# Kernel optimization log

Measured on AMD Instinct MI355X. Metric: run time of the kernel, lower is better.

The kernel has to match this reference:

```python
import jax, jax.numpy as jnp
import numpy as np

N_NODES = 10000
N_EDGES = 640000
NODE_DIM = 128
EDGE_DIM = 32
OUT_DIM = 128


def setup_inputs() -> dict:
    key = jax.random.key(0)
    k_h, k_e, k_ef, k_w1, k_w2 = jax.random.split(key, 5)
    h = jax.random.normal(k_h, (N_NODES, NODE_DIM), dtype=jnp.float32)
    edge_index = jax.random.randint(k_e, (2, N_EDGES), 0, N_NODES, dtype=jnp.int64)
    edge_features = jax.random.normal(k_ef, (N_EDGES, EDGE_DIM), dtype=jnp.float32)
    in_dim = 2 * NODE_DIM + EDGE_DIM
    # Kaiming-ish init scale for realism
    W1 = jax.random.normal(k_w1, (in_dim, OUT_DIM), dtype=jnp.float32) / np.sqrt(in_dim)
    b1 = jnp.zeros((OUT_DIM,), dtype=jnp.float32)
    W2 = jax.random.normal(k_w2, (OUT_DIM, OUT_DIM), dtype=jnp.float32) / np.sqrt(OUT_DIM)
    b2 = jnp.zeros((OUT_DIM,), dtype=jnp.float32)
    return {"h": h, "edge_index": edge_index, "edge_features": edge_features,
            "n": N_NODES, "W1": W1, "b1": b1, "W2": W2, "b2": b2}


def reference(h, edge_index, edge_features, n, W1, b1, W2, b2):
    rows, cols = edge_index[0], edge_index[1]
    # gather source/target node features + edge features -> [E, 2*node_dim+edge_dim]
    msg_input = jnp.concatenate([h[rows], h[cols], edge_features], axis=-1)
    hidden = jax.nn.relu(msg_input @ W1 + b1)   # [E, out_dim]
    messages = hidden @ W2 + b2                 # [E, out_dim]
    # scatter-add messages onto destination rows -> [n, out_dim]
    out = jax.ops.segment_sum(messages, rows, num_segments=n)
    return out
```

## Files before the change

kernel.cpp:

```cpp
#include <hip/hip_runtime.h>
#include <hip/hip_bf16.h>


typedef __attribute__((ext_vector_type(8))) short bf16x8;
typedef __attribute__((ext_vector_type(4))) float f32x4;

#define ND 128
#define ED 32
#define NL1 4096

__device__ __forceinline__ short f2bf(float x) {
  unsigned int u = __float_as_uint(x);
  unsigned int r = (u + 0x7FFFu + ((u >> 16) & 1u)) >> 16;
  return (short)r;
}

__device__ __forceinline__ float bf2f(short s) {
  return __uint_as_float(((unsigned int)(unsigned short)s) << 16);
}

__device__ __forceinline__ f32x4 bf8lo(bf16x8 v) {
  f32x4 r;
  #pragma unroll
  for (int j = 0; j < 4; ++j) r[j] = bf2f(v[j]);
  return r;
}
__device__ __forceinline__ f32x4 bf8hi(bf16x8 v) {
  f32x4 r;
  #pragma unroll
  for (int j = 0; j < 4; ++j) r[j] = bf2f(v[4 + j]);
  return r;
}

__device__ __forceinline__ int swz(int c) {
  int ct = c >> 4, cc = c & 15;
  return (ct >> 2) * 64 + (cc >> 2) * 16 + (ct & 3) * 4 + (cc & 3);
}

__global__ __launch_bounds__(256) void prep_hist_kernel(
    const float* __restrict__ W1, const float* __restrict__ W2,
    const void* __restrict__ ei, int* __restrict__ counts,
    int* __restrict__ rank, unsigned int* __restrict__ rc,
    short* __restrict__ w12t, short* __restrict__ w1eA, short* __restrict__ w2t,
    int E) {
  int b = blockIdx.x;
  if (b < 128) {
    int t = b * 256 + threadIdx.x;
    if (t < 256 * 128) {
      int np = t >> 7, k = t & 127;
      float v = (np < 128) ? W1[k * 128 + np] : W1[(128 + k) * 128 + (np - 128)];
      w12t[t] = f2bf(v);
    }
    if (t < 128 * 128) {
      int n = t >> 7, k = t & 127;
      w2t[t] = f2bf(W2[k * 128 + n]);
    }
    if (t < 8 * 64 * 8) {
      int ct = t >> 9, lane = (t >> 3) & 63, j = t & 7;
      int li = lane & 15, lg = lane >> 4;
      w1eA[t] = f2bf(W1[(256 + lg * 8 + j) * 128 + ct * 16 + li]);
    }
  } else {
    int e = (b - 128) * 256 + threadIdx.x;
    if (e < E) {
      const unsigned int* u = (const unsigned int*)ei;
      int is64 = 1;
      #pragma unroll
      for (int i = 0; i < 16; ++i)
        if (u[2 * i + 1] != 0u) is64 = 0;
      int r, c;
      if (is64) {
        r = (int)((const long long*)ei)[e];
        c = (int)((const long long*)ei)[(long long)E + e];
      } else {
        r = ((const int*)ei)[e];
        c = ((const int*)ei)[E + e];
      }
      rank[e] = atomicAdd(&counts[r], 1);
      rc[e] = ((unsigned int)r << 16) | (unsigned int)c;
    }
  }
}

__global__ __launch_bounds__(1024) void scan_kernel(const int* __restrict__ counts,
                                                    int* __restrict__ row_ptr, int n) {
  __shared__ int wtot[16];
  int tid = threadIdx.x;
  int lane = tid & 63, w = tid >> 6;
  int base_i = tid * 16;
  int c[16];
  int tot = 0;
  #pragma unroll
  for (int j = 0; j < 16; ++j) {
    int i = base_i + j;
    c[j] = (i < n) ? counts[i] : 0;
    tot += c[j];
  }
  int x = tot;
  #pragma unroll
  for (int d = 1; d < 64; d <<= 1) {
    int t = __shfl_up(x, d);
    if (lane >= d) x += t;
  }
  if (lane == 63) wtot[w] = x;
  __syncthreads();
  if (w == 0) {
    int y = (lane < 16) ? wtot[lane] : 0;
    #pragma unroll
    for (int d = 1; d < 16; d <<= 1) {
      int t = __shfl_up(y, d);
      if (lane >= d) y += t;
    }
    if (lane < 16) wtot[lane] = y;
  }
  __syncthreads();
  int waveoff = (w == 0) ? 0 : wtot[w - 1];
  int run = waveoff + x - tot;
  if (tid == 0) row_ptr[0] = 0;
  #pragma unroll
  for (int j = 0; j < 16; ++j) {
    int i = base_i + j;
    if (i < n) {
      run += c[j];
      row_ptr[i + 1] = run;
    }
  }
}

__global__ __launch_bounds__(256, 4) void scatter_sg_kernel(
    const float* __restrict__ ef, const int* __restrict__ row_ptr,
    const int* __restrict__ rank, const unsigned int* __restrict__ rc,
    const float* __restrict__ h, const short* __restrict__ w12t,
    const float* __restrict__ b1, short* __restrict__ efb,
    int* __restrict__ ccol, float* __restrict__ s2, short* __restrict__ g2,
    int N, int E) {
  int b = blockIdx.x;
  int SGB = (N + 63) >> 6;
  if (b < SGB) {
    int lane = threadIdx.x & 63, w = threadIdx.x >> 6;
    int li = lane & 15, lg = lane >> 4;
    int base = b * 64 + w * 16;
    int rowm = base + li;
    if (rowm >= N) rowm = N - 1;
    float breg[8];
    #pragma unroll
    for (int nt = 0; nt < 8; ++nt) breg[nt] = b1[nt * 16 + li];
    f32x4 acc[16];
    #pragma unroll
    for (int nt = 0; nt < 16; ++nt) acc[nt] = (f32x4){0.f, 0.f, 0.f, 0.f};
    #pragma unroll
    for (int kc = 0; kc < 4; ++kc) {
      f32x4 f0 = *(const f32x4*)(h + (size_t)rowm * ND + kc * 32 + lg * 8);
      f32x4 f1 = *(const f32x4*)(h + (size_t)rowm * ND + kc * 32 + lg * 8 + 4);
      bf16x8 a;
      #pragma unroll
      for (int j = 0; j < 4; ++j) { a[j] = f2bf(f0[j]); a[4 + j] = f2bf(f1[j]); }
      #pragma unroll
      for (int nt = 0; nt < 16; ++nt) {
        bf16x8 bb = *(const bf16x8*)(w12t + (nt * 16 + li) * 128 + kc * 32 + lg * 8);
        acc[nt] = __builtin_amdgcn_mfma_f32_16x16x32_bf16(a, bb, acc[nt], 0, 0, 0);
      }
    }
    #pragma unroll
    for (int nt = 0; nt < 16; ++nt)
      #pragma unroll
      for (int r = 0; r < 4; ++r) {
        int row = base + lg * 4 + r;
        if (row < N) {
          if (nt < 8) {
            s2[(size_t)row * 128 + swz(nt * 16 + li)] = acc[nt][r] + breg[nt];
          } else {
            g2[(size_t)row * 128 + swz((nt - 8) * 16 + li)] = f2bf(acc[nt][r]);
          }
        }
      }
  } else {
    int gt = (b - SGB) * 256 + threadIdx.x;
    int e = gt >> 2, part = gt & 3;
    if (e < E) {
      unsigned int p = rc[e];
      int r = (int)(p >> 16), c = (int)(p & 0xffffu);
      int pos = row_ptr[r] + rank[e];
      f32x4 a0 = *(const f32x4*)(ef + (size_t)e * ED + part * 8);
      f32x4 a1 = *(const f32x4*)(ef + (size_t)e * ED + part * 8 + 4);
      bf16x8 ob;
      #pragma unroll
      for (int j = 0; j < 4; ++j) { ob[j] = f2bf(a0[j]); ob[4 + j] = f2bf(a1[j]); }
      *(bf16x8*)(efb + (size_t)pos * ED + part * 8) = ob;
      if (part == 0) ccol[pos] = c;
    }
  }
}

__global__ __launch_bounds__(64) void layer1_kernel(
    const float* __restrict__ s2, const short* __restrict__ g2,
    const short* __restrict__ efb, const int* __restrict__ ccol,
    const short* __restrict__ w1eA, const int* __restrict__ row_ptr,
    float* __restrict__ hsum, int N) {
  int lane = threadIdx.x & 63;
  int li = lane & 15, lg = lane >> 4;

  bf16x8 wa[8];
  #pragma unroll
  for (int ct = 0; ct < 8; ++ct)
    wa[ct] = *(const bf16x8*)(w1eA + (ct * 64 + lane) * 8);

  for (int node = blockIdx.x; node < N; node += NL1) {
    int rp = row_ptr[node], rpe = row_ptr[node + 1];
    int deg = rpe - rp;

    if (deg == 0) {
      if (li == 0) {
        #pragma unroll
        for (int ct = 0; ct < 8; ++ct)
          *(f32x4*)(hsum + (size_t)node * 128 + ct * 16 + lg * 4) =
              (f32x4){0.f, 0.f, 0.f, 0.f};
      }
      continue;
    }

    f32x4 sreg[8];
    #pragma unroll
    for (int ct = 0; ct < 8; ++ct)
      sreg[ct] = *(const f32x4*)(s2 + (size_t)node * 128 +
                                 (ct >> 2) * 64 + lg * 16 + (ct & 3) * 4);
    f32x4 psum[8];
    #pragma unroll
    for (int ct = 0; ct < 8; ++ct) psum[ct] = (f32x4){0.f, 0.f, 0.f, 0.f};

    int ntiles = (deg + 15) >> 4;
    int last = rpe - 1;
    auto ldpos = [&](int t) {
      int p = rp + t * 16 + li;
      return p > last ? last : p;
    };

    int pA = ldpos(0), pB = ldpos(1);
    int cA = ccol[pA], cB = ccol[pB];
    bf16x8 eA = *(const bf16x8*)(efb + (size_t)pA * ED + lg * 8);
    bf16x8 eB = *(const bf16x8*)(efb + (size_t)pB * ED + lg * 8);
    const short* gpA = g2 + (size_t)cA * 128;
    bf16x8 gA0 = *(const bf16x8*)(gpA + lg * 16);
    bf16x8 gA1 = *(const bf16x8*)(gpA + lg * 16 + 8);
    bf16x8 gA2 = *(const bf16x8*)(gpA + 64 + lg * 16);
    bf16x8 gA3 = *(const bf16x8*)(gpA + 64 + lg * 16 + 8);

    for (int t = 0; t < ntiles; ++t) {
      const short* gpB = g2 + (size_t)cB * 128;
      bf16x8 gB0 = *(const bf16x8*)(gpB + lg * 16);
      bf16x8 gB1 = *(const bf16x8*)(gpB + lg * 16 + 8);
      bf16x8 gB2 = *(const bf16x8*)(gpB + 64 + lg * 16);
      bf16x8 gB3 = *(const bf16x8*)(gpB + 64 + lg * 16 + 8);
      int pC = ldpos(t + 2);
      int cC = ccol[pC];
      bf16x8 eC = *(const bf16x8*)(efb + (size_t)pC * ED + lg * 8);
      f32x4 acc[8];
      #pragma unroll
      for (int ct = 0; ct < 8; ++ct)
        acc[ct] = __builtin_amdgcn_mfma_f32_16x16x32_bf16(
            wa[ct], eA, (f32x4){0.f, 0.f, 0.f, 0.f}, 0, 0, 0);
      if ((t * 16 + li) < deg) {
        #pragma unroll
        for (int ct = 0; ct < 8; ++ct) {
          bf16x8 gr = (ct < 4) ? ((ct & 2) ? gA1 : gA0) : ((ct & 2) ? gA3 : gA2);
          f32x4 gv = (ct & 1) ? bf8hi(gr) : bf8lo(gr);
          f32x4 v = acc[ct] + sreg[ct] + gv;
          #pragma unroll
          for (int r = 0; r < 4; ++r)
            psum[ct][r] += (v[r] > 0.f ? v[r] : 0.f);
        }
      }
      cB = cC; eA = eB; eB = eC;
      gA0 = gB0; gA1 = gB1; gA2 = gB2; gA3 = gB3;
    }

    #pragma unroll
    for (int ct = 0; ct < 8; ++ct)
      #pragma unroll
      for (int r = 0; r < 4; ++r) {
        float v = psum[ct][r];
        v += __shfl_xor(v, 1);
        v += __shfl_xor(v, 2);
        v += __shfl_xor(v, 4);
        v += __shfl_xor(v, 8);
        psum[ct][r] = v;
      }
    if (li == 0) {
      #pragma unroll
      for (int ct = 0; ct < 8; ++ct)
        *(f32x4*)(hsum + (size_t)node * 128 + ct * 16 + lg * 4) = psum[ct];
    }
  }
}

__global__ __launch_bounds__(256) void out_kernel(const float* __restrict__ hsum,
                                                  const short* __restrict__ w2t,
                                                  const float* __restrict__ b2,
                                                  const int* __restrict__ row_ptr,
                                                  float* __restrict__ out, int N) {
  int lane = threadIdx.x & 63, w = threadIdx.x >> 6;
  int li = lane & 15, lg = lane >> 4;
  int base = blockIdx.x * 64 + w * 16;
  int rowm = base + li;
  if (rowm >= N) rowm = N - 1;
  float breg[8];
  #pragma unroll
  for (int nt = 0; nt < 8; ++nt) breg[nt] = b2[nt * 16 + li];
  f32x4 acc[8];
  #pragma unroll
  for (int nt = 0; nt < 8; ++nt) acc[nt] = (f32x4){0.f, 0.f, 0.f, 0.f};
  #pragma unroll
  for (int kc = 0; kc < 4; ++kc) {
    f32x4 f0 = *(const f32x4*)(hsum + (size_t)rowm * 128 + kc * 32 + lg * 8);
    f32x4 f1 = *(const f32x4*)(hsum + (size_t)rowm * 128 + kc * 32 + lg * 8 + 4);
    bf16x8 a;
    #pragma unroll
    for (int j = 0; j < 4; ++j) { a[j] = f2bf(f0[j]); a[4 + j] = f2bf(f1[j]); }
    #pragma unroll
    for (int nt = 0; nt < 8; ++nt) {
      bf16x8 bb = *(const bf16x8*)(w2t + (nt * 16 + li) * 128 + kc * 32 + lg * 8);
      acc[nt] = __builtin_amdgcn_mfma_f32_16x16x32_bf16(a, bb, acc[nt], 0, 0, 0);
    }
  }
  #pragma unroll
  for (int r = 0; r < 4; ++r) {
    int row = base + lg * 4 + r;
    if (row < N) {
      float dg = (float)(row_ptr[row + 1] - row_ptr[row]);
      #pragma unroll
      for (int nt = 0; nt < 8; ++nt)
        out[(size_t)row * 128 + nt * 16 + li] = acc[nt][r] + dg * breg[nt];
    }
  }
}

extern "C" void kernel_launch(void* const* d_in, const int* in_sizes, int n_in,
                              void* d_out, int out_size, void* d_ws, size_t ws_size,
                              hipStream_t stream) {
  const float* h  = (const float*)d_in[0];
  const void*  ei = d_in[1];
  const float* ef = (const float*)d_in[2];
  const float* W1 = (const float*)d_in[4];
  const float* b1 = (const float*)d_in[5];
  const float* W2 = (const float*)d_in[6];
  const float* b2 = (const float*)d_in[7];
  float* out = (float*)d_out;
  int N = in_sizes[0] / ND;
  int E = in_sizes[2] / ED;

  char* ws = (char*)d_ws;
  size_t off = 0;
  auto alloc = [&](size_t bytes) {
    size_t o = off;
    off = (off + bytes + 255) & ~(size_t)255;
    return o;
  };
  int*          counts  = (int*)(ws + alloc((size_t)N * 4));
  int*          row_ptr = (int*)(ws + alloc((size_t)(N + 1) * 4));
  int*          rank    = (int*)(ws + alloc((size_t)E * 4));
  unsigned int* rc      = (unsigned int*)(ws + alloc((size_t)E * 4));
  short*        w12t    = (short*)(ws + alloc(256 * 128 * 2));
  short*        w1eA    = (short*)(ws + alloc(8 * 64 * 8 * 2));
  short*        w2t     = (short*)(ws + alloc(128 * 128 * 2));
  float*        s2      = (float*)(ws + alloc((size_t)N * 128 * 4));
  short*        g2      = (short*)(ws + alloc((size_t)N * 128 * 2));
  float*        hsumb   = (float*)(ws + alloc((size_t)N * 128 * 4));
  short*        efb     = (short*)(ws + alloc((size_t)E * ED * 2));
  int*          ccol    = (int*)(ws + alloc((size_t)E * 4));

  int SGB = (N + 63) >> 6;
  int SCB = (4 * E + 255) >> 8;

  hipMemsetAsync(counts, 0, (size_t)N * 4, stream);
  prep_hist_kernel<<<128 + (E + 255) / 256, 256, 0, stream>>>(
      W1, W2, ei, counts, rank, rc, w12t, w1eA, w2t, E);
  scan_kernel<<<1, 1024, 0, stream>>>(counts, row_ptr, N);
  scatter_sg_kernel<<<SGB + SCB, 256, 0, stream>>>(
      ef, row_ptr, rank, rc, h, w12t, b1, efb, ccol, s2, g2, N, E);
  layer1_kernel<<<NL1, 64, 0, stream>>>(s2, g2, efb, ccol, w1eA, row_ptr, hsumb, N);
  out_kernel<<<(N + 63) / 64, 256, 0, stream>>>(hsumb, w2t, b2, row_ptr, out, N);
}
```

Baseline: 134.8 us.

## Fuse layer-1 edge aggregation with output matmul via shared-memory node tile

Merges the per-node layer-1 aggregation kernel and the W2 output kernel into one kernel. Each 256-thread block handles 16 nodes, four per wave, writes the summed hidden rows to LDS, and then applies W2 with MFMA, each wave covering 32 output columns. This drops the hsum global round trip and one kernel launch. In exchange, a block with uneven node degrees stalls at the barrier, and the grid changes from 4096 single-wave blocks to N/16 four-wave blocks.

```diff
diff --git a/kernel.cpp b/kernel.cpp
--- a/kernel.cpp
+++ b/kernel.cpp
@@ -7,7 +7,6 @@
 
 #define ND 128
 #define ED 32
-#define NL1 4096
 
 __device__ __forceinline__ short f2bf(float x) {
   unsigned int u = __float_as_uint(x);
@@ -192,145 +191,150 @@
   }
 }
 
-__global__ __launch_bounds__(64) void layer1_kernel(
+__global__ __launch_bounds__(256) void layer1out_kernel(
     const float* __restrict__ s2, const short* __restrict__ g2,
     const short* __restrict__ efb, const int* __restrict__ ccol,
-    const short* __restrict__ w1eA, const int* __restrict__ row_ptr,
-    float* __restrict__ hsum, int N) {
-  int lane = threadIdx.x & 63;
+    const short* __restrict__ w1eA, const short* __restrict__ w2t,
+    const float* __restrict__ b2, const int* __restrict__ row_ptr,
+    float* __restrict__ out, int N) {
+  __shared__ float hs[16][132];
+  int tid = threadIdx.x;
+  int wv = tid >> 6;
+  int lane = tid & 63;
   int li = lane & 15, lg = lane >> 4;
 
   bf16x8 wa[8];
   #pragma unroll
   for (int ct = 0; ct < 8; ++ct)
     wa[ct] = *(const bf16x8*)(w1eA + (ct * 64 + lane) * 8);
-
-  for (int node = blockIdx.x; node < N; node += NL1) {
-    int rp = row_ptr[node], rpe = row_ptr[node + 1];
-    int deg = rpe - rp;
-
-    if (deg == 0) {
+  float breg[2];
+  #pragma unroll
+  for (int nt = 0; nt < 2; ++nt) breg[nt] = b2[(wv * 2 + nt) * 16 + li];
+
+  for (int nb = blockIdx.x * 16; nb < N; nb += gridDim.x * 16) {
+    #pragma unroll 1
+    for (int i = 0; i < 4; ++i) {
+      int node = nb + wv * 4 + i;
+      int lrow = wv * 4 + i;
+      if (node >= N) {
+        if (li == 0) {
+          #pragma unroll
+          for (int ct = 0; ct < 8; ++ct)
+            *(f32x4*)(&hs[lrow][ct * 16 + lg * 4]) = (f32x4){0.f, 0.f, 0.f, 0.f};
+        }
+        continue;
+      }
+      int rp = row_ptr[node], rpe = row_ptr[node + 1];
+      int deg = rpe - rp;
+      if (deg == 0) {
+        if (li == 0) {
+          #pragma unroll
+          for (int ct = 0; ct < 8; ++ct)
+            *(f32x4*)(&hs[lrow][ct * 16 + lg * 4]) = (f32x4){0.f, 0.f, 0.f, 0.f};
+        }
+        continue;
+      }
+
+      f32x4 sreg[8];
+      #pragma unroll
+      for (int ct = 0; ct < 8; ++ct)
+        sreg[ct] = *(const f32x4*)(s2 + (size_t)node * 128 +
+                                   (ct >> 2) * 64 + lg * 16 + (ct & 3) * 4);
+      f32x4 psum[8];
+      #pragma unroll
+      for (int ct = 0; ct < 8; ++ct) psum[ct] = (f32x4){0.f, 0.f, 0.f, 0.f};
+
+      int ntiles = (deg + 15) >> 4;
+      int last = rpe - 1;
+      auto ldpos = [&](int t) {
+        int p = rp + t * 16 + li;
+        return p > last ? last : p;
+      };
+
+      int pA = ldpos(0), pB = ldpos(1);
+      int cA = ccol[pA], cB = ccol[pB];
+      bf16x8 eA = *(const bf16x8*)(efb + (size_t)pA * ED + lg * 8);
+      bf16x8 eB = *(const bf16x8*)(efb + (size_t)pB * ED + lg * 8);
+      const short* gpA = g2 + (size_t)cA * 128;
+      bf16x8 gA0 = *(const bf16x8*)(gpA + lg * 16);
+      bf16x8 gA1 = *(const bf16x8*)(gpA + lg * 16 + 8);
+      bf16x8 gA2 = *(const bf16x8*)(gpA + 64 + lg * 16);
+      bf16x8 gA3 = *(const bf16x8*)(gpA + 64 + lg * 16 + 8);
+
+      for (int t = 0; t < ntiles; ++t) {
+        const short* gpB = g2 + (size_t)cB * 128;
+        bf16x8 gB0 = *(const bf16x8*)(gpB + lg * 16);
+        bf16x8 gB1 = *(const bf16x8*)(gpB + lg * 16 + 8);
+        bf16x8 gB2 = *(const bf16x8*)(gpB + 64 + lg * 16);
+        bf16x8 gB3 = *(const bf16x8*)(gpB + 64 + lg * 16 + 8);
+        int pC = ldpos(t + 2);
+        int cC = ccol[pC];
+        bf16x8 eC = *(const bf16x8*)(efb + (size_t)pC * ED + lg * 8);
+        f32x4 acc[8];
+        #pragma unroll
+        for (int ct = 0; ct < 8; ++ct)
+          acc[ct] = __builtin_amdgcn_mfma_f32_16x16x32_bf16(
+              wa[ct], eA, (f32x4){0.f, 0.f, 0.f, 0.f}, 0, 0, 0);
+        if ((t * 16 + li) < deg) {
+          #pragma unroll
+          for (int ct = 0; ct < 8; ++ct) {
+            bf16x8 gr = (ct < 4) ? ((ct & 2) ? gA1 : gA0) : ((ct & 2) ? gA3 : gA2);
+            f32x4 gv = (ct & 1) ? bf8hi(gr) : bf8lo(gr);
+            f32x4 v = acc[ct] + sreg[ct] + gv;
+            #pragma unroll
+            for (int r = 0; r < 4; ++r)
+              psum[ct][r] += (v[r] > 0.f ? v[r] : 0.f);
+          }
+        }
+        cB = cC; eA = eB; eB = eC;
+        gA0 = gB0; gA1 = gB1; gA2 = gB2; gA3 = gB3;
+      }
+
+      #pragma unroll
+      for (int ct = 0; ct < 8; ++ct)
+        #pragma unroll
+        for (int r = 0; r < 4; ++r) {
+          float v = psum[ct][r];
+          v += __shfl_xor(v, 1);
+          v += __shfl_xor(v, 2);
+          v += __shfl_xor(v, 4);
+          v += __shfl_xor(v, 8);
+          psum[ct][r] = v;
+        }
       if (li == 0) {
         #pragma unroll
         for (int ct = 0; ct < 8; ++ct)
-          *(f32x4*)(hsum + (size_t)node * 128 + ct * 16 + lg * 4) =
-              (f32x4){0.f, 0.f, 0.f, 0.f};
-      }
-      continue;
-    }
-
-    f32x4 sreg[8];
-    #pragma unroll
-    for (int ct = 0; ct < 8; ++ct)
-      sreg[ct] = *(const f32x4*)(s2 + (size_t)node * 128 +
-                                 (ct >> 2) * 64 + lg * 16 + (ct & 3) * 4);
-    f32x4 psum[8];
-    #pragma unroll
-    for (int ct = 0; ct < 8; ++ct) psum[ct] = (f32x4){0.f, 0.f, 0.f, 0.f};
-
-    int ntiles = (deg + 15) >> 4;
-    int last = rpe - 1;
-    auto ldpos = [&](int t) {
-      int p = rp + t * 16 + li;
-      return p > last ? last : p;
-    };
-
-    int pA = ldpos(0), pB = ldpos(1);
-    int cA = ccol[pA], cB = ccol[pB];
-    bf16x8 eA = *(const bf16x8*)(efb + (size_t)pA * ED + lg * 8);
-    bf16x8 eB = *(const bf16x8*)(efb + (size_t)pB * ED + lg * 8);
-    const short* gpA = g2 + (size_t)cA * 128;
-    bf16x8 gA0 = *(const bf16x8*)(gpA + lg * 16);
-    bf16x8 gA1 = *(const bf16x8*)(gpA + lg * 16 + 8);
-    bf16x8 gA2 = *(const bf16x8*)(gpA + 64 + lg * 16);
-    bf16x8 gA3 = *(const bf16x8*)(gpA + 64 + lg * 16 + 8);
-
-    for (int t = 0; t < ntiles; ++t) {
-      const short* gpB = g2 + (size_t)cB * 128;
-      bf16x8 gB0 = *(const bf16x8*)(gpB + lg * 16);
-      bf16x8 gB1 = *(const bf16x8*)(gpB + lg * 16 + 8);
-      bf16x8 gB2 = *(const bf16x8*)(gpB + 64 + lg * 16);
-      bf16x8 gB3 = *(const bf16x8*)(gpB + 64 + lg * 16 + 8);
-      int pC = ldpos(t + 2);
-      int cC = ccol[pC];
-      bf16x8 eC = *(const bf16x8*)(efb + (size_t)pC * ED + lg * 8);
-      f32x4 acc[8];
-      #pragma unroll
-      for (int ct = 0; ct < 8; ++ct)
-        acc[ct] = __builtin_amdgcn_mfma_f32_16x16x32_bf16(
-            wa[ct], eA, (f32x4){0.f, 0.f, 0.f, 0.f}, 0, 0, 0);
-      if ((t * 16 + li) < deg) {
+          *(f32x4*)(&hs[lrow][ct * 16 + lg * 4]) = psum[ct];
+      }
+    }
+    __syncthreads();
+
+    f32x4 oacc[2];
+    #pragma unroll
+    for (int nt = 0; nt < 2; ++nt) oacc[nt] = (f32x4){0.f, 0.f, 0.f, 0.f};
+    #pragma unroll
+    for (int kc = 0; kc < 4; ++kc) {
+      bf16x8 a;
+      #pragma unroll
+      for (int j = 0; j < 8; ++j) a[j] = f2bf(hs[li][kc * 32 + lg * 8 + j]);
+      #pragma unroll
+      for (int nt = 0; nt < 2; ++nt) {
+        bf16x8 bb = *(const bf16x8*)(w2t + ((wv * 2 + nt) * 16 + li) * 128 +
+                                     kc * 32 + lg * 8);
+        oacc[nt] = __builtin_amdgcn_mfma_f32_16x16x32_bf16(a, bb, oacc[nt], 0, 0, 0);
+      }
+    }
+    #pragma unroll
+    for (int r = 0; r < 4; ++r) {
+      int row = nb + lg * 4 + r;
+      if (row < N) {
+        float dg = (float)(row_ptr[row + 1] - row_ptr[row]);
         #pragma unroll
-        for (int ct = 0; ct < 8; ++ct) {
-          bf16x8 gr = (ct < 4) ? ((ct & 2) ? gA1 : gA0) : ((ct & 2) ? gA3 : gA2);
-          f32x4 gv = (ct & 1) ? bf8hi(gr) : bf8lo(gr);
-          f32x4 v = acc[ct] + sreg[ct] + gv;
-          #pragma unroll
-          for (int r = 0; r < 4; ++r)
-            psum[ct][r] += (v[r] > 0.f ? v[r] : 0.f);
-        }
-      }
-      cB = cC; eA = eB; eB = eC;
-      gA0 = gB0; gA1 = gB1; gA2 = gB2; gA3 = gB3;
-    }
-
-    #pragma unroll
-    for (int ct = 0; ct < 8; ++ct)
-      #pragma unroll
-      for (int r = 0; r < 4; ++r) {
-        float v = psum[ct][r];
-        v += __shfl_xor(v, 1);
-        v += __shfl_xor(v, 2);
-        v += __shfl_xor(v, 4);
-        v += __shfl_xor(v, 8);
-        psum[ct][r] = v;
-      }
-    if (li == 0) {
-      #pragma unroll
-      for (int ct = 0; ct < 8; ++ct)
-        *(f32x4*)(hsum + (size_t)node * 128 + ct * 16 + lg * 4) = psum[ct];
-    }
-  }
-}
-
-__global__ __launch_bounds__(256) void out_kernel(const float* __restrict__ hsum,
-                                                  const short* __restrict__ w2t,
-                                                  const float* __restrict__ b2,
-                                                  const int* __restrict__ row_ptr,
-                                                  float* __restrict__ out, int N) {
-  int lane = threadIdx.x & 63, w = threadIdx.x >> 6;
-  int li = lane & 15, lg = lane >> 4;
-  int base = blockIdx.x * 64 + w * 16;
-  int rowm = base + li;
-  if (rowm >= N) rowm = N - 1;
-  float breg[8];
-  #pragma unroll
-  for (int nt = 0; nt < 8; ++nt) breg[nt] = b2[nt * 16 + li];
-  f32x4 acc[8];
-  #pragma unroll
-  for (int nt = 0; nt < 8; ++nt) acc[nt] = (f32x4){0.f, 0.f, 0.f, 0.f};
-  #pragma unroll
-  for (int kc = 0; kc < 4; ++kc) {
-    f32x4 f0 = *(const f32x4*)(hsum + (size_t)rowm * 128 + kc * 32 + lg * 8);
-    f32x4 f1 = *(const f32x4*)(hsum + (size_t)rowm * 128 + kc * 32 + lg * 8 + 4);
-    bf16x8 a;
-    #pragma unroll
-    for (int j = 0; j < 4; ++j) { a[j] = f2bf(f0[j]); a[4 + j] = f2bf(f1[j]); }
-    #pragma unroll
-    for (int nt = 0; nt < 8; ++nt) {
-      bf16x8 bb = *(const bf16x8*)(w2t + (nt * 16 + li) * 128 + kc * 32 + lg * 8);
-      acc[nt] = __builtin_amdgcn_mfma_f32_16x16x32_bf16(a, bb, acc[nt], 0, 0, 0);
-    }
-  }
-  #pragma unroll
-  for (int r = 0; r < 4; ++r) {
-    int row = base + lg * 4 + r;
-    if (row < N) {
-      float dg = (float)(row_ptr[row + 1] - row_ptr[row]);
-      #pragma unroll
-      for (int nt = 0; nt < 8; ++nt)
-        out[(size_t)row * 128 + nt * 16 + li] = acc[nt][r] + dg * breg[nt];
-    }
+        for (int nt = 0; nt < 2; ++nt)
+          out[(size_t)row * 128 + (wv * 2 + nt) * 16 + li] = oacc[nt][r] + dg * breg[nt];
+      }
+    }
+    __syncthreads();
   }
 }
 
@@ -364,12 +368,12 @@
   short*        w2t     = (short*)(ws + alloc(128 * 128 * 2));
   float*        s2      = (float*)(ws + alloc((size_t)N * 128 * 4));
   short*        g2      = (short*)(ws + alloc((size_t)N * 128 * 2));
-  float*        hsumb   = (float*)(ws + alloc((size_t)N * 128 * 4));
   short*        efb     = (short*)(ws + alloc((size_t)E * ED * 2));
   int*          ccol    = (int*)(ws + alloc((size_t)E * 4));
 
   int SGB = (N + 63) >> 6;
   int SCB = (4 * E + 255) >> 8;
+  int NLB = (N + 15) >> 4;
 
   hipMemsetAsync(counts, 0, (size_t)N * 4, stream);
   prep_hist_kernel<<<128 + (E + 255) / 256, 256, 0, stream>>>(
@@ -377,6 +381,6 @@
   scan_kernel<<<1, 1024, 0, stream>>>(counts, row_ptr, N);
   scatter_sg_kernel<<<SGB + SCB, 256, 0, stream>>>(
       ef, row_ptr, rank, rc, h, w12t, b1, efb, ccol, s2, g2, N, E);
-  layer1_kernel<<<NL1, 64, 0, stream>>>(s2, g2, efb, ccol, w1eA, row_ptr, hsumb, N);
-  out_kernel<<<(N + 63) / 64, 256, 0, stream>>>(hsumb, w2t, b2, row_ptr, out, N);
-}
+  layer1out_kernel<<<NLB, 256, 0, stream>>>(
+      s2, g2, efb, ccol, w1eA, w2t, b2, row_ptr, out, N);
+}
```

After: 155.7 us. +15.5%, slower.
